# Optimization experiments

Hardware: AMD Instinct MI355X
Metric: run time of the kernel (lower is better)

The kernel has to match this reference:

```python
import jax, jax.numpy as jnp
import numpy as np

N_NODES = 100000
N_EDGES = 300000
F = 256


def setup_inputs() -> dict:
    key = jax.random.key(0)
    k1, k2, k3, k4, k5, k6 = jax.random.split(key, 6)
    x = jax.random.normal(k1, (N_NODES, F), dtype=jnp.float32)
    edge_index = jax.random.randint(k2, (2, N_EDGES), 0, N_NODES, dtype=jnp.int32)
    # GCNConv learned params (PyG: lin weight [out,in] applied as x @ W.T; store as [in,out])
    W_conv = jax.random.normal(k3, (F, F), dtype=jnp.float32) / np.sqrt(F)
    b_conv = jax.random.normal(k4, (F,), dtype=jnp.float32) * 0.01
    W_lin = jax.random.normal(k5, (F, 1), dtype=jnp.float32) / np.sqrt(F)
    b_lin = jax.random.normal(k6, (1,), dtype=jnp.float32) * 0.01
    return {"x": x, "edge_index": edge_index, "W_conv": W_conv,
            "b_conv": b_conv, "W_lin": W_lin, "b_lin": b_lin}


def gcn_conv(x, edge_index, W_conv, b_conv):
    N = x.shape[0]
    # add self loops (PyG default add_self_loops=True)
    loop = jnp.arange(N, dtype=edge_index.dtype)
    src = jnp.concatenate([edge_index[0], loop])
    dst = jnp.concatenate([edge_index[1], loop])
    # symmetric normalization: deg over destination, norm = d^-1/2[src]*d^-1/2[dst]
    deg = jax.ops.segment_sum(jnp.ones_like(dst, dtype=x.dtype), dst, num_segments=N)
    dinv = jnp.where(deg > 0, jax.lax.rsqrt(deg), 0.0)
    norm = dinv[src] * dinv[dst]  # [E+N]
    h = x @ W_conv  # [N,F] dense transform first (PyG order)
    msg = h[src] * norm[:, None]  # gather + scale, [E+N, F]
    agg = jax.ops.segment_sum(msg, dst, num_segments=N)  # scatter-add, [N,F]
    return agg + b_conv


def reference(x, edge_index, W_conv, b_conv, W_lin, b_lin):
    h = jax.nn.relu(gcn_conv(x, edge_index, W_conv, b_conv))
    return jax.nn.sigmoid(h @ W_lin + b_lin)  # [N,1]
```

## Files before the change

### kernel.cpp

```cpp
#include <hip/hip_runtime.h>
#include <hip/hip_bf16.h>
#include <math.h>

#define FDIM 256

typedef short bfrag __attribute__((ext_vector_type(8)));
typedef float f32x4 __attribute__((ext_vector_type(4)));

__device__ __forceinline__ short f2bf_rne(float f) {
    uint32_t u = __float_as_uint(f);
    uint32_t r = (u + 0x7FFFu + ((u >> 16) & 1u)) >> 16;
    return (short)r;
}
__device__ __forceinline__ float bf2f(unsigned short s) {
    return __uint_as_float(((uint32_t)s) << 16);
}

#define GLOAD_LDS16(g, l) __builtin_amdgcn_global_load_lds(              \
    (const __attribute__((address_space(1))) void*)(g),                  \
    (__attribute__((address_space(3))) void*)(l), 16, 0, 0)

__global__ void count_kernel(const int* __restrict__ dst, int* __restrict__ counts, int E) {
    int e = blockIdx.x * 256 + threadIdx.x;
    if (e < E) atomicAdd(&counts[dst[e]], 1);
}

__global__ void scan1_kernel(const int* __restrict__ counts, int* __restrict__ blksums, int N) {
    __shared__ int sd[256];
    int tid = threadIdx.x;
    int base = blockIdx.x * 1024 + tid * 4;
    int s = 0;
#pragma unroll
    for (int t = 0; t < 4; ++t) { int i = base + t; if (i < N) s += counts[i]; }
    sd[tid] = s; __syncthreads();
    for (int off = 128; off > 0; off >>= 1) {
        if (tid < off) sd[tid] += sd[tid + off];
        __syncthreads();
    }
    if (tid == 0) blksums[blockIdx.x] = sd[0];
}

__global__ void scan2_kernel(int* __restrict__ blksums, int NB) {
    __shared__ int sd[128];
    int tid = threadIdx.x;
    int v = (tid < NB) ? blksums[tid] : 0;
    sd[tid] = v; __syncthreads();
    for (int off = 1; off < 128; off <<= 1) {
        int t = (tid >= off) ? sd[tid - off] : 0;
        __syncthreads();
        sd[tid] += t;
        __syncthreads();
    }
    if (tid < NB) blksums[tid] = sd[tid] - v;
}

__global__ void scan3_kernel(const int* __restrict__ counts, const int* __restrict__ blksums,
                             int* __restrict__ offsets, int* __restrict__ cursor,
                             float* __restrict__ dinv, int N, int E) {
    __shared__ int sd[256];
    int tid = threadIdx.x;
    int base = blockIdx.x * 1024 + tid * 4;
    int c[4]; int s = 0;
#pragma unroll
    for (int t = 0; t < 4; ++t) { int i = base + t; c[t] = (i < N) ? counts[i] : 0; s += c[t]; }
    sd[tid] = s; __syncthreads();
    int v = s;
    for (int off = 1; off < 256; off <<= 1) {
        int t = (tid >= off) ? sd[tid - off] : 0;
        __syncthreads();
        sd[tid] += t;
        __syncthreads();
    }
    int run = sd[tid] - v + blksums[blockIdx.x];
#pragma unroll
    for (int t = 0; t < 4; ++t) {
        int i = base + t;
        if (i < N) {
            offsets[i] = run;
            cursor[i]  = run;
            dinv[i] = rsqrtf((float)(c[t] + 1));
            run += c[t];
        }
    }
    if (blockIdx.x == 0 && tid == 0) offsets[N] = E;
}

__global__ void fill_kernel(const int* __restrict__ src, const int* __restrict__ dst,
                            int* __restrict__ cursor, const float* __restrict__ dinv,
                            int* __restrict__ csr_src, float* __restrict__ csr_norm, int E) {
    int e = blockIdx.x * 256 + threadIdx.x;
    if (e < E) {
        int s = src[e], d = dst[e];
        int pos = atomicAdd(&cursor[d], 1);
        csr_src[pos]  = s;
        csr_norm[pos] = dinv[s] * dinv[d];
    }
}

__global__ void wsplit_kernel(const float* __restrict__ W,
                              short* __restrict__ Wh, short* __restrict__ Wl) {
    const int k = blockIdx.x;
    const int n = threadIdx.x;
    const float w = W[k * 256 + n];
    const short hi = f2bf_rne(w);
    const short lo = f2bf_rne(w - bf2f((unsigned short)hi));
    const int s = k >> 5, g = (k & 31) >> 3, j = k & 7;
    const size_t idx = (size_t)s * 8192 + n * 32 + g * 8 + j;
    Wh[idx] = hi; Wl[idx] = lo;
}

__global__ __launch_bounds__(512) void gemm_mfma(const float* __restrict__ X,
                                                 const short* __restrict__ Wth,
                                                 const short* __restrict__ Wtl,
                                                 unsigned short* __restrict__ Hb, int N) {
    __shared__ short Xh[2][4096], Xl[2][4096];
    __shared__ short Wh[2][8192], Wl[2][8192];

    const int tid  = threadIdx.x;
    const int lane = tid & 63;
    const int wid  = tid >> 6;
    const int wm   = wid >> 2;
    const int wn   = wid & 3;
    const int row0 = blockIdx.x * 128;
    const int sm   = tid >> 2;
    const int g    = lane >> 4;
    const int r15  = lane & 15;

    f32x4 acc[4][4];
#pragma unroll
    for (int i = 0; i < 4; ++i)
#pragma unroll
        for (int j = 0; j < 4; ++j) acc[i][j] = (f32x4){0.f, 0.f, 0.f, 0.f};

    const int xrow = row0 + sm;
    const float* xbase = X + (size_t)xrow * FDIM + 8 * (tid & 3);

    float4 xa0, xa1;
    if (xrow < N) { xa0 = *(const float4*)xbase; xa1 = *(const float4*)(xbase + 4); }
    else          { xa0 = make_float4(0,0,0,0); xa1 = make_float4(0,0,0,0); }
    {
        const float v[8] = {xa0.x,xa0.y,xa0.z,xa0.w,xa1.x,xa1.y,xa1.z,xa1.w};
        bfrag hi8, lo8;
#pragma unroll
        for (int j = 0; j < 8; ++j) {
            const short h = f2bf_rne(v[j]);
            hi8[j] = h; lo8[j] = f2bf_rne(v[j] - bf2f((unsigned short)h));
        }
        *(bfrag*)(&Xh[0][tid * 8]) = hi8;
        *(bfrag*)(&Xl[0][tid * 8]) = lo8;
    }
#pragma unroll
    for (int p = 0; p < 2; ++p) {
        GLOAD_LDS16(Wth + p * 4096 + wid * 512 + lane * 8, &Wh[0][p * 4096 + wid * 512]);
        GLOAD_LDS16(Wtl + p * 4096 + wid * 512 + lane * 8, &Wl[0][p * 4096 + wid * 512]);
    }
    if (xrow < N) { xa0 = *(const float4*)(xbase + 32); xa1 = *(const float4*)(xbase + 36); }
    else          { xa0 = make_float4(0,0,0,0); xa1 = make_float4(0,0,0,0); }
    __syncthreads();

    for (int s = 0; s < 8; ++s) {
        const int cur = s & 1, nxt = cur ^ 1;
        if (s < 7) {
            const float v[8] = {xa0.x,xa0.y,xa0.z,xa0.w,xa1.x,xa1.y,xa1.z,xa1.w};
            bfrag hi8, lo8;
#pragma unroll
            for (int j = 0; j < 8; ++j) {
                const short h = f2bf_rne(v[j]);
                hi8[j] = h; lo8[j] = f2bf_rne(v[j] - bf2f((unsigned short)h));
            }
            *(bfrag*)(&Xh[nxt][tid * 8]) = hi8;
            *(bfrag*)(&Xl[nxt][tid * 8]) = lo8;
            const short* gh = Wth + (s + 1) * 8192;
            const short* gl = Wtl + (s + 1) * 8192;
#pragma unroll
            for (int p = 0; p < 2; ++p) {
                GLOAD_LDS16(gh + p * 4096 + wid * 512 + lane * 8, &Wh[nxt][p * 4096 + wid * 512]);
                GLOAD_LDS16(gl + p * 4096 + wid * 512 + lane * 8, &Wl[nxt][p * 4096 + wid * 512]);
            }
        }
        if (s < 6) {
            if (xrow < N) {
                const float* src = xbase + (s + 2) * 32;
                xa0 = *(const float4*)src; xa1 = *(const float4*)(src + 4);
            } else { xa0 = make_float4(0,0,0,0); xa1 = make_float4(0,0,0,0); }
        }

        bfrag bh[4], bl[4];
#pragma unroll
        for (int ni = 0; ni < 4; ++ni) {
            const int off = ((wn * 64 + ni * 16 + r15) * 4 + g) * 8;
            bh[ni] = *(const bfrag*)(&Wh[cur][off]);
            bl[ni] = *(const bfrag*)(&Wl[cur][off]);
        }
#pragma unroll
        for (int mi = 0; mi < 4; ++mi) {
            const int off = ((wm * 64 + mi * 16 + r15) * 4 + g) * 8;
            const bfrag ah = *(const bfrag*)(&Xh[cur][off]);
            const bfrag al = *(const bfrag*)(&Xl[cur][off]);
#pragma unroll
            for (int ni = 0; ni < 4; ++ni) {
                acc[mi][ni] = __builtin_amdgcn_mfma_f32_16x16x32_bf16(ah, bh[ni], acc[mi][ni], 0, 0, 0);
                acc[mi][ni] = __builtin_amdgcn_mfma_f32_16x16x32_bf16(ah, bl[ni], acc[mi][ni], 0, 0, 0);
                acc[mi][ni] = __builtin_amdgcn_mfma_f32_16x16x32_bf16(al, bh[ni], acc[mi][ni], 0, 0, 0);
            }
        }
        if (s < 7) __syncthreads();
    }

#pragma unroll
    for (int mi = 0; mi < 4; ++mi) {
        const int rowb = row0 + wm * 64 + mi * 16 + g * 4;
#pragma unroll
        for (int r = 0; r < 4; ++r) {
            const int row = rowb + r;
            if (row < N) {
                unsigned short* base = Hb + (size_t)row * FDIM + wn * 64 + r15;
#pragma unroll
                for (int ni = 0; ni < 4; ++ni)
                    base[ni * 16] = (unsigned short)f2bf_rne(acc[mi][ni][r]);
            }
        }
    }
}

__global__ __launch_bounds__(256) void agg_kernel(const unsigned short* __restrict__ hb,
                                                  const int* __restrict__ offsets,
                                                  const int* __restrict__ csr_src,
                                                  const float* __restrict__ csr_norm,
                                                  const float* __restrict__ dinv,
                                                  const float* __restrict__ b_conv,
                                                  const float* __restrict__ W_lin,
                                                  const float* __restrict__ b_lin,
                                                  float* __restrict__ out, int N) {
    const int wid  = threadIdx.x >> 6;
    const int lane = threadIdx.x & 63;
    const int node = blockIdx.x * 4 + wid;
    if (node >= N) return;

    float a0 = 0.f, a1 = 0.f, a2 = 0.f, a3 = 0.f;
    float c0 = 0.f, c1 = 0.f, c2 = 0.f, c3 = 0.f;

    const int start = offsets[node];
    const int end   = offsets[node + 1];
    const float di  = dinv[node];

    int j = start;
    for (; j + 1 < end; j += 2) {
        const int   s0 = csr_src[j],     s1 = csr_src[j + 1];
        const float w0 = csr_norm[j],    w1 = csr_norm[j + 1];
        const ushort4 v0 = *((const ushort4*)(hb + (size_t)s0 * FDIM) + lane);
        const ushort4 v1 = *((const ushort4*)(hb + (size_t)s1 * FDIM) + lane);
        a0 = fmaf(bf2f(v0.x), w0, a0); a1 = fmaf(bf2f(v0.y), w0, a1);
        a2 = fmaf(bf2f(v0.z), w0, a2); a3 = fmaf(bf2f(v0.w), w0, a3);
        c0 = fmaf(bf2f(v1.x), w1, c0); c1 = fmaf(bf2f(v1.y), w1, c1);
        c2 = fmaf(bf2f(v1.z), w1, c2); c3 = fmaf(bf2f(v1.w), w1, c3);
    }
    if (j < end) {
        const int   s0 = csr_src[j];
        const float w0 = csr_norm[j];
        const ushort4 v0 = *((const ushort4*)(hb + (size_t)s0 * FDIM) + lane);
        a0 = fmaf(bf2f(v0.x), w0, a0); a1 = fmaf(bf2f(v0.y), w0, a1);
        a2 = fmaf(bf2f(v0.z), w0, a2); a3 = fmaf(bf2f(v0.w), w0, a3);
    }
    {
        const float w = di * di;
        const ushort4 v = *((const ushort4*)(hb + (size_t)node * FDIM) + lane);
        a0 = fmaf(bf2f(v.x), w, a0); a1 = fmaf(bf2f(v.y), w, a1);
        a2 = fmaf(bf2f(v.z), w, a2); a3 = fmaf(bf2f(v.w), w, a3);
    }
    a0 += c0; a1 += c1; a2 += c2; a3 += c3;

    const float4 bc = ((const float4*)b_conv)[lane];
    a0 = fmaxf(a0 + bc.x, 0.f); a1 = fmaxf(a1 + bc.y, 0.f);
    a2 = fmaxf(a2 + bc.z, 0.f); a3 = fmaxf(a3 + bc.w, 0.f);

    const float4 wl = ((const float4*)W_lin)[lane];
    float p = a0 * wl.x + a1 * wl.y + a2 * wl.z + a3 * wl.w;
#pragma unroll
    for (int off = 32; off > 0; off >>= 1) p += __shfl_xor(p, off);
    if (lane == 0) out[node] = 1.f / (1.f + expf(-(p + b_lin[0])));
}

extern "C" void kernel_launch(void* const* d_in, const int* in_sizes, int n_in,
                              void* d_out, int out_size, void* d_ws, size_t ws_size,
                              hipStream_t stream) {
    const float* x      = (const float*)d_in[0];
    const int*   eidx   = (const int*)d_in[1];
    const float* W_conv = (const float*)d_in[2];
    const float* b_conv = (const float*)d_in[3];
    const float* W_lin  = (const float*)d_in[4];
    const float* b_lin  = (const float*)d_in[5];
    float* out = (float*)d_out;

    const int N = in_sizes[0] / FDIM;
    const int E = in_sizes[1] / 2;
    const int* e_src = eidx;
    const int* e_dst = eidx + E;

    char* p = (char*)d_ws;
    unsigned short* hb = (unsigned short*)p; p += (size_t)N * FDIM * sizeof(unsigned short);
    int* counts   = (int*)p;        p += (size_t)N * sizeof(int);
    int* offsets  = (int*)p;        p += (size_t)(N + 1) * sizeof(int);
    int* cursor   = (int*)p;        p += (size_t)N * sizeof(int);
    float* dinv   = (float*)p;      p += (size_t)N * sizeof(float);
    int* csr_src  = (int*)p;        p += (size_t)E * sizeof(int);
    float* csr_norm = (float*)p;    p += (size_t)E * sizeof(float);
    int* blksums  = (int*)p;        p += 128 * sizeof(int);
    short* Wth    = (short*)p;      p += (size_t)FDIM * FDIM * sizeof(short);
    short* Wtl    = (short*)p;      p += (size_t)FDIM * FDIM * sizeof(short);

    const int NB = (N + 1023) / 1024;

    hipMemsetAsync(counts, 0, (size_t)N * sizeof(int), stream);

    count_kernel<<<(E + 255) / 256, 256, 0, stream>>>(e_dst, counts, E);
    scan1_kernel<<<NB, 256, 0, stream>>>(counts, blksums, N);
    scan2_kernel<<<1, 128, 0, stream>>>(blksums, NB);
    scan3_kernel<<<NB, 256, 0, stream>>>(counts, blksums, offsets, cursor, dinv, N, E);
    fill_kernel<<<(E + 255) / 256, 256, 0, stream>>>(e_src, e_dst, cursor, dinv,
                                                     csr_src, csr_norm, E);

    wsplit_kernel<<<FDIM, FDIM, 0, stream>>>(W_conv, Wth, Wtl);

    gemm_mfma<<<(N + 127) / 128, 512, 0, stream>>>(x, Wth, Wtl, hb, N);

    agg_kernel<<<(N + 3) / 4, 256, 0, stream>>>(hb, offsets, csr_src, csr_norm, dinv,
                                                b_conv, W_lin, b_lin, out, N);
}
```

Before: 286.8 us.

## Fold source-side dinv into GEMM epilogue, drop csr_norm, shrink GEMM tile

The GEMM epilogue now scales each output row by dinv[row], so aggregation only needs an unweighted sum over neighbours followed by one multiply by the destination dinv. This removes the csr_norm array, its writes in fill_kernel and its reads in aggregation. The GEMM row tile drops from 128 to 64 rows per block with a min-occupancy launch bound, and the MFMA calls are regrouped by hi/lo term. Aggregation now uses 16 lanes per node with 16-byte loads and processes one edge per iteration instead of two. This trades less memory traffic and more parallelism for reuse of W across fewer rows per block and less unrolling in the edge loop.

New measurement: 269.2 us. -6.1%, faster.

```diff
diff --git a/kernel.cpp b/kernel.cpp
--- a/kernel.cpp
+++ b/kernel.cpp
@@ -5,7 +5,9 @@
 #define FDIM 256
 
 typedef short bfrag __attribute__((ext_vector_type(8)));
+typedef short s16x4 __attribute__((ext_vector_type(4)));
 typedef float f32x4 __attribute__((ext_vector_type(4)));
+typedef unsigned short u16x8 __attribute__((ext_vector_type(8)));
 
 __device__ __forceinline__ short f2bf_rne(float f) {
     uint32_t u = __float_as_uint(f);
@@ -86,14 +88,12 @@
 }
 
 __global__ void fill_kernel(const int* __restrict__ src, const int* __restrict__ dst,
-                            int* __restrict__ cursor, const float* __restrict__ dinv,
-                            int* __restrict__ csr_src, float* __restrict__ csr_norm, int E) {
+                            int* __restrict__ cursor, int* __restrict__ csr_src, int E) {
     int e = blockIdx.x * 256 + threadIdx.x;
     if (e < E) {
         int s = src[e], d = dst[e];
         int pos = atomicAdd(&cursor[d], 1);
-        csr_src[pos]  = s;
-        csr_norm[pos] = dinv[s] * dinv[d];
+        csr_src[pos] = s;
     }
 }
 
@@ -109,11 +109,12 @@
     Wh[idx] = hi; Wl[idx] = lo;
 }
 
-__global__ __launch_bounds__(512) void gemm_mfma(const float* __restrict__ X,
-                                                 const short* __restrict__ Wth,
-                                                 const short* __restrict__ Wtl,
-                                                 unsigned short* __restrict__ Hb, int N) {
-    __shared__ short Xh[2][4096], Xl[2][4096];
+__global__ __launch_bounds__(512, 4) void gemm_mfma(const float* __restrict__ X,
+                                                    const short* __restrict__ Wth,
+                                                    const short* __restrict__ Wtl,
+                                                    const float* __restrict__ dinv,
+                                                    unsigned short* __restrict__ Hb, int N) {
+    __shared__ short Xh[2][2048], Xl[2][2048];
     __shared__ short Wh[2][8192], Wl[2][8192];
 
     const int tid  = threadIdx.x;
@@ -121,71 +122,73 @@
     const int wid  = tid >> 6;
     const int wm   = wid >> 2;
     const int wn   = wid & 3;
-    const int row0 = blockIdx.x * 128;
-    const int sm   = tid >> 2;
+    const int row0 = blockIdx.x * 64;
     const int g    = lane >> 4;
     const int r15  = lane & 15;
 
-    f32x4 acc[4][4];
-#pragma unroll
-    for (int i = 0; i < 4; ++i)
+    const int srow = tid >> 3, skq = tid & 7;
+    const int sg = skq >> 1, sj = (skq & 1) * 4;
+    const int xoff = (srow * 4 + sg) * 8 + sj;
+    const int xrow = row0 + srow;
+    const float* xptr = X + (size_t)xrow * FDIM + skq * 4;
+
+    f32x4 acc[2][4];
+#pragma unroll
+    for (int i = 0; i < 2; ++i)
 #pragma unroll
         for (int j = 0; j < 4; ++j) acc[i][j] = (f32x4){0.f, 0.f, 0.f, 0.f};
 
-    const int xrow = row0 + sm;
-    const float* xbase = X + (size_t)xrow * FDIM + 8 * (tid & 3);
-
-    float4 xa0, xa1;
-    if (xrow < N) { xa0 = *(const float4*)xbase; xa1 = *(const float4*)(xbase + 4); }
-    else          { xa0 = make_float4(0,0,0,0); xa1 = make_float4(0,0,0,0); }
+    float4 xa;
+    xa = (xrow < N) ? *(const float4*)xptr : make_float4(0, 0, 0, 0);
     {
-        const float v[8] = {xa0.x,xa0.y,xa0.z,xa0.w,xa1.x,xa1.y,xa1.z,xa1.w};
-        bfrag hi8, lo8;
-#pragma unroll
-        for (int j = 0; j < 8; ++j) {
+        const float v[4] = {xa.x, xa.y, xa.z, xa.w};
+        s16x4 hi4, lo4;
+#pragma unroll
+        for (int j = 0; j < 4; ++j) {
             const short h = f2bf_rne(v[j]);
-            hi8[j] = h; lo8[j] = f2bf_rne(v[j] - bf2f((unsigned short)h));
-        }
-        *(bfrag*)(&Xh[0][tid * 8]) = hi8;
-        *(bfrag*)(&Xl[0][tid * 8]) = lo8;
+            hi4[j] = h; lo4[j] = f2bf_rne(v[j] - bf2f((unsigned short)h));
+        }
+        *(s16x4*)(&Xh[0][xoff]) = hi4;
+        *(s16x4*)(&Xl[0][xoff]) = lo4;
     }
 #pragma unroll
     for (int p = 0; p < 2; ++p) {
-        GLOAD_LDS16(Wth + p * 4096 + wid * 512 + lane * 8, &Wh[0][p * 4096 + wid * 512]);
-        GLOAD_LDS16(Wtl + p * 4096 + wid * 512 + lane * 8, &Wl[0][p * 4096 + wid * 512]);
-    }
-    if (xrow < N) { xa0 = *(const float4*)(xbase + 32); xa1 = *(const float4*)(xbase + 36); }
-    else          { xa0 = make_float4(0,0,0,0); xa1 = make_float4(0,0,0,0); }
+        GLOAD_LDS16(Wth + p * 4096 + tid * 8, &Wh[0][p * 4096 + tid * 8]);
+        GLOAD_LDS16(Wtl + p * 4096 + tid * 8, &Wl[0][p * 4096 + tid * 8]);
+    }
+    xa = (xrow < N) ? *(const float4*)(xptr + 32) : make_float4(0, 0, 0, 0);
     __syncthreads();
 
     for (int s = 0; s < 8; ++s) {
         const int cur = s & 1, nxt = cur ^ 1;
         if (s < 7) {
-            const float v[8] = {xa0.x,xa0.y,xa0.z,xa0.w,xa1.x,xa1.y,xa1.z,xa1.w};
-            bfrag hi8, lo8;
-#pragma unroll
-            for (int j = 0; j < 8; ++j) {
+            const float v[4] = {xa.x, xa.y, xa.z, xa.w};
+            s16x4 hi4, lo4;
+#pragma unroll
+            for (int j = 0; j < 4; ++j) {
                 const short h = f2bf_rne(v[j]);
-                hi8[j] = h; lo8[j] = f2bf_rne(v[j] - bf2f((unsigned short)h));
+                hi4[j] = h; lo4[j] = f2bf_rne(v[j] - bf2f((unsigned short)h));
             }
-            *(bfrag*)(&Xh[nxt][tid * 8]) = hi8;
-            *(bfrag*)(&Xl[nxt][tid * 8]) = lo8;
+            *(s16x4*)(&Xh[nxt][xoff]) = hi4;
+            *(s16x4*)(&Xl[nxt][xoff]) = lo4;
             const short* gh = Wth + (s + 1) * 8192;
             const short* gl = Wtl + (s + 1) * 8192;
 #pragma unroll
             for (int p = 0; p < 2; ++p) {
-                GLOAD_LDS16(gh + p * 4096 + wid * 512 + lane * 8, &Wh[nxt][p * 4096 + wid * 512]);
-                GLOAD_LDS16(gl + p * 4096 + wid * 512 + lane * 8, &Wl[nxt][p * 4096 + wid * 512]);
+                GLOAD_LDS16(gh + p * 4096 + tid * 8, &Wh[nxt][p * 4096 + tid * 8]);
+                GLOAD_LDS16(gl + p * 4096 + tid * 8, &Wl[nxt][p * 4096 + tid * 8]);
             }
         }
-        if (s < 6) {
-            if (xrow < N) {
-                const float* src = xbase + (s + 2) * 32;
-                xa0 = *(const float4*)src; xa1 = *(const float4*)(src + 4);
-            } else { xa0 = make_float4(0,0,0,0); xa1 = make_float4(0,0,0,0); }
-        }
-
-        bfrag bh[4], bl[4];
+        if (s < 6)
+            xa = (xrow < N) ? *(const float4*)(xptr + (s + 2) * 32) : make_float4(0, 0, 0, 0);
+
+        bfrag ah[2], al[2], bh[4], bl[4];
+#pragma unroll
+        for (int mi = 0; mi < 2; ++mi) {
+            const int off = ((wm * 32 + mi * 16 + r15) * 4 + g) * 8;
+            ah[mi] = *(const bfrag*)(&Xh[cur][off]);
+            al[mi] = *(const bfrag*)(&Xl[cur][off]);
+        }
 #pragma unroll
         for (int ni = 0; ni < 4; ++ni) {
             const int off = ((wn * 64 + ni * 16 + r15) * 4 + g) * 8;
@@ -193,31 +196,36 @@
             bl[ni] = *(const bfrag*)(&Wl[cur][off]);
         }
 #pragma unroll
-        for (int mi = 0; mi < 4; ++mi) {
-            const int off = ((wm * 64 + mi * 16 + r15) * 4 + g) * 8;
-            const bfrag ah = *(const bfrag*)(&Xh[cur][off]);
-            const bfrag al = *(const bfrag*)(&Xl[cur][off]);
-#pragma unroll
-            for (int ni = 0; ni < 4; ++ni) {
-                acc[mi][ni] = __builtin_amdgcn_mfma_f32_16x16x32_bf16(ah, bh[ni], acc[mi][ni], 0, 0, 0);
-                acc[mi][ni] = __builtin_amdgcn_mfma_f32_16x16x32_bf16(ah, bl[ni], acc[mi][ni], 0, 0, 0);
-                acc[mi][ni] = __builtin_amdgcn_mfma_f32_16x16x32_bf16(al, bh[ni], acc[mi][ni], 0, 0, 0);
-            }
-        }
+        for (int mi = 0; mi < 2; ++mi)
+#pragma unroll
+            for (int ni = 0; ni < 4; ++ni)
+                acc[mi][ni] = __builtin_amdgcn_mfma_f32_16x16x32_bf16(ah[mi], bh[ni], acc[mi][ni], 0, 0, 0);
+#pragma unroll
+        for (int mi = 0; mi < 2; ++mi)
+#pragma unroll
+            for (int ni = 0; ni < 4; ++ni)
+                acc[mi][ni] = __builtin_amdgcn_mfma_f32_16x16x32_bf16(ah[mi], bl[ni], acc[mi][ni], 0, 0, 0);
+#pragma unroll
+        for (int mi = 0; mi < 2; ++mi)
+#pragma unroll
+            for (int ni = 0; ni < 4; ++ni)
+                acc[mi][ni] = __builtin_amdgcn_mfma_f32_16x16x32_bf16(al[mi], bh[ni], acc[mi][ni], 0, 0, 0);
+
         if (s < 7) __syncthreads();
     }
 
 #pragma unroll
-    for (int mi = 0; mi < 4; ++mi) {
-        const int rowb = row0 + wm * 64 + mi * 16 + g * 4;
+    for (int mi = 0; mi < 2; ++mi) {
+        const int rowb = row0 + wm * 32 + mi * 16 + g * 4;
 #pragma unroll
         for (int r = 0; r < 4; ++r) {
             const int row = rowb + r;
             if (row < N) {
+                const float dv = dinv[row];
                 unsigned short* base = Hb + (size_t)row * FDIM + wn * 64 + r15;
 #pragma unroll
                 for (int ni = 0; ni < 4; ++ni)
-                    base[ni * 16] = (unsigned short)f2bf_rne(acc[mi][ni][r]);
+                    base[ni * 16] = (unsigned short)f2bf_rne(acc[mi][ni][r] * dv);
             }
         }
     }
@@ -226,59 +234,47 @@
 __global__ __launch_bounds__(256) void agg_kernel(const unsigned short* __restrict__ hb,
                                                   const int* __restrict__ offsets,
                                                   const int* __restrict__ csr_src,
-                                                  const float* __restrict__ csr_norm,
                                                   const float* __restrict__ dinv,
                                                   const float* __restrict__ b_conv,
                                                   const float* __restrict__ W_lin,
                                                   const float* __restrict__ b_lin,
                                                   float* __restrict__ out, int N) {
-    const int wid  = threadIdx.x >> 6;
-    const int lane = threadIdx.x & 63;
-    const int node = blockIdx.x * 4 + wid;
+    const int t    = threadIdx.x;
+    const int l16  = t & 15;
+    const int node = blockIdx.x * 16 + (t >> 4);
     if (node >= N) return;
-
-    float a0 = 0.f, a1 = 0.f, a2 = 0.f, a3 = 0.f;
-    float c0 = 0.f, c1 = 0.f, c2 = 0.f, c3 = 0.f;
 
     const int start = offsets[node];
     const int end   = offsets[node + 1];
-    const float di  = dinv[node];
-
-    int j = start;
-    for (; j + 1 < end; j += 2) {
-        const int   s0 = csr_src[j],     s1 = csr_src[j + 1];
-        const float w0 = csr_norm[j],    w1 = csr_norm[j + 1];
-        const ushort4 v0 = *((const ushort4*)(hb + (size_t)s0 * FDIM) + lane);
-        const ushort4 v1 = *((const ushort4*)(hb + (size_t)s1 * FDIM) + lane);
-        a0 = fmaf(bf2f(v0.x), w0, a0); a1 = fmaf(bf2f(v0.y), w0, a1);
-        a2 = fmaf(bf2f(v0.z), w0, a2); a3 = fmaf(bf2f(v0.w), w0, a3);
-        c0 = fmaf(bf2f(v1.x), w1, c0); c1 = fmaf(bf2f(v1.y), w1, c1);
-        c2 = fmaf(bf2f(v1.z), w1, c2); c3 = fmaf(bf2f(v1.w), w1, c3);
-    }
-    if (j < end) {
-        const int   s0 = csr_src[j];
-        const float w0 = csr_norm[j];
-        const ushort4 v0 = *((const ushort4*)(hb + (size_t)s0 * FDIM) + lane);
-        a0 = fmaf(bf2f(v0.x), w0, a0); a1 = fmaf(bf2f(v0.y), w0, a1);
-        a2 = fmaf(bf2f(v0.z), w0, a2); a3 = fmaf(bf2f(v0.w), w0, a3);
-    }
+
+    float acc[16];
     {
-        const float w = di * di;
-        const ushort4 v = *((const ushort4*)(hb + (size_t)node * FDIM) + lane);
-        a0 = fmaf(bf2f(v.x), w, a0); a1 = fmaf(bf2f(v.y), w, a1);
-        a2 = fmaf(bf2f(v.z), w, a2); a3 = fmaf(bf2f(v.w), w, a3);
-    }
-    a0 += c0; a1 += c1; a2 += c2; a3 += c3;
-
-    const float4 bc = ((const float4*)b_conv)[lane];
-    a0 = fmaxf(a0 + bc.x, 0.f); a1 = fmaxf(a1 + bc.y, 0.f);
-    a2 = fmaxf(a2 + bc.z, 0.f); a3 = fmaxf(a3 + bc.w, 0.f);
-
-    const float4 wl = ((const float4*)W_lin)[lane];
-    float p = a0 * wl.x + a1 * wl.y + a2 * wl.z + a3 * wl.w;
-#pragma unroll
-    for (int off = 32; off > 0; off >>= 1) p += __shfl_xor(p, off);
-    if (lane == 0) out[node] = 1.f / (1.f + expf(-(p + b_lin[0])));
+        const unsigned short* r = hb + (size_t)node * FDIM + l16 * 16;
+        const u16x8 u0 = *(const u16x8*)r, u1 = *(const u16x8*)(r + 8);
+#pragma unroll
+        for (int k = 0; k < 8; ++k) { acc[k] = bf2f(u0[k]); acc[8 + k] = bf2f(u1[k]); }
+    }
+    for (int j = start; j < end; ++j) {
+        const unsigned short* r = hb + (size_t)csr_src[j] * FDIM + l16 * 16;
+        const u16x8 u0 = *(const u16x8*)r, u1 = *(const u16x8*)(r + 8);
+#pragma unroll
+        for (int k = 0; k < 8; ++k) { acc[k] += bf2f(u0[k]); acc[8 + k] += bf2f(u1[k]); }
+    }
+
+    const float dv = dinv[node];
+    float p = 0.f;
+#pragma unroll
+    for (int q = 0; q < 4; ++q) {
+        const float4 bc = *(const float4*)(b_conv + l16 * 16 + q * 4);
+        const float4 wl = *(const float4*)(W_lin  + l16 * 16 + q * 4);
+        p = fmaf(fmaxf(fmaf(acc[q * 4 + 0], dv, bc.x), 0.f), wl.x, p);
+        p = fmaf(fmaxf(fmaf(acc[q * 4 + 1], dv, bc.y), 0.f), wl.y, p);
+        p = fmaf(fmaxf(fmaf(acc[q * 4 + 2], dv, bc.z), 0.f), wl.z, p);
+        p = fmaf(fmaxf(fmaf(acc[q * 4 + 3], dv, bc.w), 0.f), wl.w, p);
+    }
+#pragma unroll
+    for (int off = 1; off < 16; off <<= 1) p += __shfl_xor(p, off);
+    if (l16 == 0) out[node] = 1.f / (1.f + expf(-(p + b_lin[0])));
 }
 
 extern "C" void kernel_launch(void* const* d_in, const int* in_sizes, int n_in,
@@ -304,7 +300,6 @@
     int* cursor   = (int*)p;        p += (size_t)N * sizeof(int);
     float* dinv   = (float*)p;      p += (size_t)N * sizeof(float);
     int* csr_src  = (int*)p;        p += (size_t)E * sizeof(int);
-    float* csr_norm = (float*)p;    p += (size_t)E * sizeof(float);
     int* blksums  = (int*)p;        p += 128 * sizeof(int);
     short* Wth    = (short*)p;      p += (size_t)FDIM * FDIM * sizeof(short);
     short* Wtl    = (short*)p;      p += (size_t)FDIM * FDIM * sizeof(short);
@@ -317,13 +312,12 @@
     scan1_kernel<<<NB, 256, 0, stream>>>(counts, blksums, N);
     scan2_kernel<<<1, 128, 0, stream>>>(blksums, NB);
     scan3_kernel<<<NB, 256, 0, stream>>>(counts, blksums, offsets, cursor, dinv, N, E);
-    fill_kernel<<<(E + 255) / 256, 256, 0, stream>>>(e_src, e_dst, cursor, dinv,
-                                                     csr_src, csr_norm, E);
+    fill_kernel<<<(E + 255) / 256, 256, 0, stream>>>(e_src, e_dst, cursor, csr_src, E);
 
     wsplit_kernel<<<FDIM, FDIM, 0, stream>>>(W_conv, Wth, Wtl);
 
-    gemm_mfma<<<(N + 127) / 128, 512, 0, stream>>>(x, Wth, Wtl, hb, N);
-
-    agg_kernel<<<(N + 3) / 4, 256, 0, stream>>>(hb, offsets, csr_src, csr_norm, dinv,
-                                                b_conv, W_lin, b_lin, out, N);
-}
+    gemm_mfma<<<(N + 63) / 64, 512, 0, stream>>>(x, Wth, Wtl, dinv, hb, N);
+
+    agg_kernel<<<(N + 15) / 16, 256, 0, stream>>>(hb, offsets, csr_src, dinv,
+                                                  b_conv, W_lin, b_lin, out, N);
+}
```
